# Optimization experiments

Hardware: AMD Instinct MI355X
Metric: run time of the kernel (lower is better)

Reference implementation:

```python
import jax, jax.numpy as jnp
import numpy as np

N_NODES = 22  # hardcoded EEG electrode count in the original module
K = 3         # Chebyshev / hop order


def setup_inputs() -> dict:
    key = jax.random.key(0)
    k1, k2, k3 = jax.random.split(key, 3)
    B, T, E = 256, 500, 40  # batch, seq_len (in=out features), emb_size
    x = jax.random.normal(k1, (B, N_NODES, T), jnp.float32)
    adj = jax.random.normal(k2, (N_NODES, N_NODES), jnp.float32)      # learnable adjacency logits
    W = jax.random.normal(k3, (K, T, T), jnp.float32) * 0.02          # per-hop feature transform
    b = jnp.zeros((T,), jnp.float32)
    return {"x": x, "adj": adj, "W": W, "b": b, "emb_size": E}


def reference(x, adj, W, b, emb_size):
    # x: (B, 22, T). K-hop graph convolution with learnable normalized adjacency:
    #   out = sum_k (A^k x) @ W[k] + b
    A = jax.nn.softmax(adj, axis=-1)                     # (22, 22) row-normalized
    h = x
    out = jnp.einsum('bnt,to->bno', h, W[0])
    for k in range(1, K):
        h = jnp.einsum('nm,bmt->bnt', A, h)              # propagate one hop
        out = out + jnp.einsum('bnt,to->bno', h, W[k])
    out = out + b                                        # (B, 22, T)
    # The original runs the SAME graph_conv emb_size times and stacks on dim 1;
    # all copies are identical, so compute once and tile.
    return jnp.tile(out[:, None], (1, emb_size, 1, 1))   # (B, emb_size, 22, T)
```

## Files before the change

kernel.cpp:

```cpp
#include <hip/hip_runtime.h>
#include <hip/hip_bf16.h>
#include <math.h>

#define N_NODES 22
#define T_DIM   500
#define TP      512
#define KHOP    3
#define KK      (KHOP*TP)
#define MROWS   5632
#define SLICE   (N_NODES*T_DIM)
#define SLICE4  (SLICE/4)
#define NS      3

typedef __bf16 v8bf __attribute__((ext_vector_type(8)));
typedef float  v4f  __attribute__((ext_vector_type(4)));

__global__ __launch_bounds__(512) void prep_adj(const float* __restrict__ adj,
                                                float* __restrict__ A1,
                                                float* __restrict__ A2) {
    __shared__ float As[N_NODES][N_NODES];
    int tid = threadIdx.x;
    if (tid < N_NODES) {
        float row[N_NODES];
        float m = -1e30f;
        for (int j = 0; j < N_NODES; ++j) { row[j] = adj[tid*N_NODES + j]; m = fmaxf(m, row[j]); }
        float s = 0.f;
        for (int j = 0; j < N_NODES; ++j) { row[j] = expf(row[j] - m); s += row[j]; }
        float inv = 1.f / s;
        for (int j = 0; j < N_NODES; ++j) { float v = row[j]*inv; As[tid][j] = v; A1[tid*N_NODES + j] = v; }
    }
    __syncthreads();
    if (tid < N_NODES*N_NODES) {
        int n = tid / N_NODES, mm = tid - (tid / N_NODES)*N_NODES;
        float s = 0.f;
        for (int k = 0; k < N_NODES; ++k) s += As[n][k] * As[k][mm];
        A2[tid] = s;
    }
}

__global__ __launch_bounds__(256) void prep_W(const float* __restrict__ W,
                                              __hip_bfloat16* __restrict__ Wt) {
    __shared__ float tile[64][65];
    const int tb = blockIdx.x * 64, ob = blockIdx.y * 64, k = blockIdx.z;
    const int tx = threadIdx.x & 63;
    const int ty = threadIdx.x >> 6;
#pragma unroll
    for (int r = ty; r < 64; r += 4) {
        int t = tb + r, o = ob + tx;
        tile[r][tx] = (t < T_DIM && o < T_DIM) ? W[(size_t)k*T_DIM*T_DIM + (size_t)t*T_DIM + o] : 0.f;
    }
    __syncthreads();
#pragma unroll
    for (int r = ty; r < 64; r += 4) {
        int o = ob + r, t = tb + tx;
        Wt[(size_t)o*KK + (size_t)k*TP + t] = __float2bfloat16(tile[tx][r]);
    }
}

__global__ __launch_bounds__(256) void prep_H(const float* __restrict__ x,
                                              const float* __restrict__ A1,
                                              const float* __restrict__ A2,
                                              __hip_bfloat16* __restrict__ Hb) {
    __shared__ float xs[N_NODES][256];
    __shared__ float A1s[N_NODES*N_NODES];
    __shared__ float A2s[N_NODES*N_NODES];
    const int b = blockIdx.x, t0 = blockIdx.y * 256, tid = threadIdx.x;
    for (int idx = tid; idx < N_NODES*256; idx += 256) {
        int n = idx >> 8, t = idx & 255;
        int tg = t0 + t;
        xs[n][t] = (tg < T_DIM) ? x[((size_t)b*N_NODES + n)*T_DIM + tg] : 0.f;
    }
    for (int idx = tid; idx < N_NODES*N_NODES; idx += 256) { A1s[idx] = A1[idx]; A2s[idx] = A2[idx]; }
    __syncthreads();
    const int t = tid;
    for (int n = 0; n < N_NODES; ++n) {
        float h0 = xs[n][t];
        float h1 = 0.f, h2 = 0.f;
        for (int m = 0; m < N_NODES; ++m) {
            float xv = xs[m][t];
            h1 = fmaf(A1s[n*N_NODES + m], xv, h1);
            h2 = fmaf(A2s[n*N_NODES + m], xv, h2);
        }
        size_t base = ((size_t)b*N_NODES + n)*KK + t0 + t;
        Hb[base]        = __float2bfloat16(h0);
        Hb[base + TP]   = __float2bfloat16(h1);
        Hb[base + 2*TP] = __float2bfloat16(h2);
    }
}

#define BM 64
#define BN 64
#define BK 64
#define NT (KK/BK)

__global__ __launch_bounds__(256) void gemm_compact(const __hip_bfloat16* __restrict__ Hb,
                                                    const __hip_bfloat16* __restrict__ Wt,
                                                    const float* __restrict__ bias,
                                                    float* __restrict__ out, int E) {
    __shared__ __hip_bfloat16 sA[2][BM*BK];
    __shared__ __hip_bfloat16 sB[2][BN*BK];
    const int tid  = threadIdx.x;
    const int bn   = blockIdx.x;
    const int bm   = blockIdx.y;
    const int lane = tid & 63, wid = tid >> 6;
    const int wr = wid >> 1, wc = wid & 1;

    const int row0_ = tid >> 3,           c0_ = tid & 7;
    const int row1_ = (tid + 256) >> 3,   c1_ = tid & 7;
    const int sOffA0 = (row0_*8 + (c0_ ^ (row0_ & 7)))*8;
    const int sOffA1 = (row1_*8 + (c1_ ^ (row1_ & 7)))*8;

    const size_t a_base = (size_t)(bm*BM) * KK;
    const size_t b_base = (size_t)(bn*BN) * KK;
    const __hip_bfloat16* gA0 = Hb + a_base + (size_t)row0_*KK + c0_*8;
    const __hip_bfloat16* gA1 = Hb + a_base + (size_t)row1_*KK + c1_*8;
    const __hip_bfloat16* gB0 = Wt + b_base + (size_t)row0_*KK + c0_*8;
    const __hip_bfloat16* gB1 = Wt + b_base + (size_t)row1_*KK + c1_*8;

    v4f acc[2][2];
#pragma unroll
    for (int m = 0; m < 2; ++m)
#pragma unroll
        for (int n = 0; n < 2; ++n) acc[m][n] = (v4f){0.f, 0.f, 0.f, 0.f};

    int aOff[2], bOff[2][2];
#pragma unroll
    for (int m = 0; m < 2; ++m) {
        int row = wr*32 + m*16 + (lane & 15);
        aOff[m] = row*8;
    }

    uint4 na0 = *(const uint4*)gA0;
    uint4 na1 = *(const uint4*)gA1;
    uint4 nb0 = *(const uint4*)gB0;
    uint4 nb1 = *(const uint4*)gB1;

    int cur = 0;
    for (int t = 0; t < NT; ++t) {
        *(uint4*)(sA[cur] + sOffA0) = na0;
        *(uint4*)(sA[cur] + sOffA1) = na1;
        *(uint4*)(sB[cur] + sOffA0) = nb0;
        *(uint4*)(sB[cur] + sOffA1) = nb1;
        __syncthreads();

        if (t + 1 < NT) {
            int k1 = (t + 1) * BK;
            na0 = *(const uint4*)(gA0 + k1);
            na1 = *(const uint4*)(gA1 + k1);
            nb0 = *(const uint4*)(gB0 + k1);
            nb1 = *(const uint4*)(gB1 + k1);
        }

#pragma unroll
        for (int ks = 0; ks < 2; ++ks) {
            v8bf af[2], bfr[2];
#pragma unroll
            for (int m = 0; m < 2; ++m) {
                int row = wr*32 + m*16 + (lane & 15);
                int c   = ks*4 + (lane >> 4);
                af[m] = *(const v8bf*)(sA[cur] + (row*8 + (c ^ (row & 7)))*8);
            }
#pragma unroll
            for (int n = 0; n < 2; ++n) {
                int row = wc*32 + n*16 + (lane & 15);
                int c   = ks*4 + (lane >> 4);
                bfr[n] = *(const v8bf*)(sB[cur] + (row*8 + (c ^ (row & 7)))*8);
            }
#pragma unroll
            for (int m = 0; m < 2; ++m)
#pragma unroll
                for (int n = 0; n < 2; ++n)
                    acc[m][n] = __builtin_amdgcn_mfma_f32_16x16x32_bf16(af[m], bfr[n], acc[m][n], 0, 0, 0);
        }
        cur ^= 1;
    }

    const int row0 = bm*BM + wr*32;
    const int col0 = bn*BN + wc*32;
#pragma unroll
    for (int n = 0; n < 2; ++n) {
        int col = col0 + n*16 + (lane & 15);
        if (col >= T_DIM) continue;
        float bv = bias[col];
#pragma unroll
        for (int m = 0; m < 2; ++m) {
            int rowb = row0 + m*16 + ((lane >> 4) << 2);
#pragma unroll
            for (int r = 0; r < 4; ++r) {
                int row  = rowb + r;
                int bidx = row / N_NODES;
                int node = row - bidx*N_NODES;
                out[((size_t)bidx*E*N_NODES + node)*T_DIM + col] = acc[m][n][r] + bv;
            }
        }
    }
}

__global__ __launch_bounds__(256) void bcast3(float* __restrict__ out, int E) {
    const int b = blockIdx.x;
    const int g = blockIdx.y;
    const v4f* __restrict__ src = (const v4f*)(out + (size_t)b*E*SLICE);
    v4f vals[11];
#pragma unroll
    for (int c = 0; c < 11; ++c) {
        int i = (int)threadIdx.x + c*256;
        if (i < SLICE4) vals[c] = src[i];
    }
    const int e0 = 1 + g*NS;
#pragma unroll
    for (int e = 0; e < NS; ++e) {
        v4f* __restrict__ dst = (v4f*)(out + ((size_t)b*E + e0 + e)*SLICE);
#pragma unroll
        for (int c = 0; c < 11; ++c) {
            int i = (int)threadIdx.x + c*256;
            if (i < SLICE4) dst[i] = vals[c];
        }
    }
}

extern "C" void kernel_launch(void* const* d_in, const int* in_sizes, int n_in,
                              void* d_out, int out_size, void* d_ws, size_t ws_size,
                              hipStream_t stream) {
    const float* x    = (const float*)d_in[0];
    const float* adj  = (const float*)d_in[1];
    const float* W    = (const float*)d_in[2];
    const float* bias = (const float*)d_in[3];
    const int B = in_sizes[0] / (N_NODES * T_DIM);
    const int E = out_size / (B * N_NODES * T_DIM);

    char* ws = (char*)d_ws;
    float* A1 = (float*)ws;
    float* A2 = A1 + 512;
    __hip_bfloat16* Wt = (__hip_bfloat16*)(ws + 4096);
    __hip_bfloat16* Hb = (__hip_bfloat16*)(ws + 4096 + (size_t)TP*KK*2);
    float* out = (float*)d_out;

    prep_adj<<<1, 512, 0, stream>>>(adj, A1, A2);
    prep_W<<<dim3(8, 8, KHOP), 256, 0, stream>>>(W, Wt);
    dim3 hg(B, 2);
    prep_H<<<hg, 256, 0, stream>>>(x, A1, A2, Hb);
    dim3 grid(8, (B*N_NODES)/BM);
    gemm_compact<<<grid, 256, 0, stream>>>(Hb, Wt, bias, out, E);
    if (E > 1) {
        dim3 bg(B, (E - 1 + NS - 1) / NS);
        bcast3<<<bg, 256, 0, stream>>>(out, E);
    }
}
```

Before: 152.2 us.

## Fuse adjacency, weight and feature prep into one kernel; widen broadcast per block

Merges the three preprocessing kernels (softmax adjacency, weight transpose/convert, hop features) into a single launch. Each H block recomputes the softmax and A^2 in shared memory, and extra blocks handle the W transpose. This removes two launches and the serialized single-block adjacency kernel, at the cost of redundant small per-block compute. The broadcast kernel now writes 6 copies per block instead of 3, with an added bound check, so fewer blocks each do more stores.

```diff
diff --git a/kernel.cpp b/kernel.cpp
--- a/kernel.cpp
+++ b/kernel.cpp
@@ -10,81 +10,79 @@
 #define MROWS   5632
 #define SLICE   (N_NODES*T_DIM)
 #define SLICE4  (SLICE/4)
-#define NS      3
+#define NS      6
 
 typedef __bf16 v8bf __attribute__((ext_vector_type(8)));
 typedef float  v4f  __attribute__((ext_vector_type(4)));
 
-__global__ __launch_bounds__(512) void prep_adj(const float* __restrict__ adj,
-                                                float* __restrict__ A1,
-                                                float* __restrict__ A2) {
-    __shared__ float As[N_NODES][N_NODES];
-    int tid = threadIdx.x;
-    if (tid < N_NODES) {
-        float row[N_NODES];
-        float m = -1e30f;
-        for (int j = 0; j < N_NODES; ++j) { row[j] = adj[tid*N_NODES + j]; m = fmaxf(m, row[j]); }
-        float s = 0.f;
-        for (int j = 0; j < N_NODES; ++j) { row[j] = expf(row[j] - m); s += row[j]; }
-        float inv = 1.f / s;
-        for (int j = 0; j < N_NODES; ++j) { float v = row[j]*inv; As[tid][j] = v; A1[tid*N_NODES + j] = v; }
-    }
-    __syncthreads();
-    if (tid < N_NODES*N_NODES) {
-        int n = tid / N_NODES, mm = tid - (tid / N_NODES)*N_NODES;
-        float s = 0.f;
-        for (int k = 0; k < N_NODES; ++k) s += As[n][k] * As[k][mm];
-        A2[tid] = s;
-    }
-}
-
-__global__ __launch_bounds__(256) void prep_W(const float* __restrict__ W,
-                                              __hip_bfloat16* __restrict__ Wt) {
-    __shared__ float tile[64][65];
-    const int tb = blockIdx.x * 64, ob = blockIdx.y * 64, k = blockIdx.z;
-    const int tx = threadIdx.x & 63;
-    const int ty = threadIdx.x >> 6;
-#pragma unroll
-    for (int r = ty; r < 64; r += 4) {
-        int t = tb + r, o = ob + tx;
-        tile[r][tx] = (t < T_DIM && o < T_DIM) ? W[(size_t)k*T_DIM*T_DIM + (size_t)t*T_DIM + o] : 0.f;
-    }
-    __syncthreads();
-#pragma unroll
-    for (int r = ty; r < 64; r += 4) {
-        int o = ob + r, t = tb + tx;
-        Wt[(size_t)o*KK + (size_t)k*TP + t] = __float2bfloat16(tile[tx][r]);
-    }
-}
-
-__global__ __launch_bounds__(256) void prep_H(const float* __restrict__ x,
-                                              const float* __restrict__ A1,
-                                              const float* __restrict__ A2,
-                                              __hip_bfloat16* __restrict__ Hb) {
-    __shared__ float xs[N_NODES][256];
-    __shared__ float A1s[N_NODES*N_NODES];
-    __shared__ float A2s[N_NODES*N_NODES];
-    const int b = blockIdx.x, t0 = blockIdx.y * 256, tid = threadIdx.x;
-    for (int idx = tid; idx < N_NODES*256; idx += 256) {
-        int n = idx >> 8, t = idx & 255;
-        int tg = t0 + t;
-        xs[n][t] = (tg < T_DIM) ? x[((size_t)b*N_NODES + n)*T_DIM + tg] : 0.f;
-    }
-    for (int idx = tid; idx < N_NODES*N_NODES; idx += 256) { A1s[idx] = A1[idx]; A2s[idx] = A2[idx]; }
-    __syncthreads();
-    const int t = tid;
-    for (int n = 0; n < N_NODES; ++n) {
-        float h0 = xs[n][t];
-        float h1 = 0.f, h2 = 0.f;
-        for (int m = 0; m < N_NODES; ++m) {
-            float xv = xs[m][t];
-            h1 = fmaf(A1s[n*N_NODES + m], xv, h1);
-            h2 = fmaf(A2s[n*N_NODES + m], xv, h2);
-        }
-        size_t base = ((size_t)b*N_NODES + n)*KK + t0 + t;
-        Hb[base]        = __float2bfloat16(h0);
-        Hb[base + TP]   = __float2bfloat16(h1);
-        Hb[base + 2*TP] = __float2bfloat16(h2);
+__global__ __launch_bounds__(256) void prep_all(const float* __restrict__ x,
+                                                const float* __restrict__ adj,
+                                                const float* __restrict__ W,
+                                                __hip_bfloat16* __restrict__ Hb,
+                                                __hip_bfloat16* __restrict__ Wt, int B) {
+    __shared__ __align__(16) char smem[26624];
+    const int bid = blockIdx.x, tid = threadIdx.x;
+
+    if (bid < 2*B) {
+        float (*xs)[256] = (float(*)[256])smem;
+        float* As  = (float*)(smem + 22528);
+        float* A2s = (float*)(smem + 24464);
+        const int b = bid >> 1, t0 = (bid & 1) * 256;
+
+        for (int idx = tid; idx < N_NODES*256; idx += 256) {
+            int n = idx >> 8, t = idx & 255;
+            int tg = t0 + t;
+            xs[n][t] = (tg < T_DIM) ? x[((size_t)b*N_NODES + n)*T_DIM + tg] : 0.f;
+        }
+        if (tid < N_NODES) {
+            float row[N_NODES];
+            float m = -1e30f;
+            for (int j = 0; j < N_NODES; ++j) { row[j] = adj[tid*N_NODES + j]; m = fmaxf(m, row[j]); }
+            float s = 0.f;
+            for (int j = 0; j < N_NODES; ++j) { row[j] = expf(row[j] - m); s += row[j]; }
+            float inv = 1.f / s;
+            for (int j = 0; j < N_NODES; ++j) As[tid*N_NODES + j] = row[j]*inv;
+        }
+        __syncthreads();
+        for (int idx = tid; idx < N_NODES*N_NODES; idx += 256) {
+            int n = idx / N_NODES, mm = idx - n*N_NODES;
+            float s = 0.f;
+            for (int k = 0; k < N_NODES; ++k) s += As[n*N_NODES + k] * As[k*N_NODES + mm];
+            A2s[idx] = s;
+        }
+        __syncthreads();
+        const int t = tid;
+        for (int n = 0; n < N_NODES; ++n) {
+            float h0 = xs[n][t];
+            float h1 = 0.f, h2 = 0.f;
+            for (int m = 0; m < N_NODES; ++m) {
+                float xv = xs[m][t];
+                h1 = fmaf(As[n*N_NODES + m],  xv, h1);
+                h2 = fmaf(A2s[n*N_NODES + m], xv, h2);
+            }
+            size_t base = ((size_t)b*N_NODES + n)*KK + t0 + t;
+            Hb[base]        = __float2bfloat16(h0);
+            Hb[base + TP]   = __float2bfloat16(h1);
+            Hb[base + 2*TP] = __float2bfloat16(h2);
+        }
+    } else {
+        float (*tile)[65] = (float(*)[65])smem;
+        const int widx = bid - 2*B;
+        const int k = widx >> 6;
+        const int rem = widx & 63;
+        const int tb = (rem & 7) * 64, ob = (rem >> 3) * 64;
+        const int tx = tid & 63, ty = tid >> 6;
+#pragma unroll
+        for (int r = ty; r < 64; r += 4) {
+            int t = tb + r, o = ob + tx;
+            tile[r][tx] = (t < T_DIM && o < T_DIM) ? W[(size_t)k*T_DIM*T_DIM + (size_t)t*T_DIM + o] : 0.f;
+        }
+        __syncthreads();
+#pragma unroll
+        for (int r = ty; r < 64; r += 4) {
+            int o = ob + r, t = tb + tx;
+            Wt[(size_t)o*KK + (size_t)k*TP + t] = __float2bfloat16(tile[tx][r]);
+        }
     }
 }
 
@@ -123,13 +121,6 @@
 #pragma unroll
         for (int n = 0; n < 2; ++n) acc[m][n] = (v4f){0.f, 0.f, 0.f, 0.f};
 
-    int aOff[2], bOff[2][2];
-#pragma unroll
-    for (int m = 0; m < 2; ++m) {
-        int row = wr*32 + m*16 + (lane & 15);
-        aOff[m] = row*8;
-    }
-
     uint4 na0 = *(const uint4*)gA0;
     uint4 na1 = *(const uint4*)gA1;
     uint4 nb0 = *(const uint4*)gB0;
@@ -209,6 +200,7 @@
     const int e0 = 1 + g*NS;
 #pragma unroll
     for (int e = 0; e < NS; ++e) {
+        if (e0 + e >= E) break;
         v4f* __restrict__ dst = (v4f*)(out + ((size_t)b*E + e0 + e)*SLICE);
 #pragma unroll
         for (int c = 0; c < 11; ++c) {
@@ -229,16 +221,11 @@
     const int E = out_size / (B * N_NODES * T_DIM);
 
     char* ws = (char*)d_ws;
-    float* A1 = (float*)ws;
-    float* A2 = A1 + 512;
-    __hip_bfloat16* Wt = (__hip_bfloat16*)(ws + 4096);
-    __hip_bfloat16* Hb = (__hip_bfloat16*)(ws + 4096 + (size_t)TP*KK*2);
+    __hip_bfloat16* Wt = (__hip_bfloat16*)ws;
+    __hip_bfloat16* Hb = (__hip_bfloat16*)(ws + (size_t)TP*KK*2);
     float* out = (float*)d_out;
 
-    prep_adj<<<1, 512, 0, stream>>>(adj, A1, A2);
-    prep_W<<<dim3(8, 8, KHOP), 256, 0, stream>>>(W, Wt);
-    dim3 hg(B, 2);
-    prep_H<<<hg, 256, 0, stream>>>(x, A1, A2, Hb);
+    prep_all<<<2*B + 192, 256, 0, stream>>>(x, adj, W, Hb, Wt, B);
     dim3 grid(8, (B*N_NODES)/BM);
     gemm_compact<<<grid, 256, 0, stream>>>(Hb, Wt, bias, out, E);
     if (E > 1) {
```

New measurement: 138.8 us. 8.8% less time.
